# Optimization experiments

Measured on AMD Instinct MI355X. Metric: run time of the kernel, lower is better.

The kernel has to match this reference:

```python
import jax, jax.numpy as jnp
from jax import lax
import numpy as np

HIDDEN = 16
INPUT = 1
OUTPUT = 1
BATCH = 8192
SEQ = 512


def setup_inputs() -> dict:
    key = jax.random.key(0)
    ks = jax.random.split(key, 12)
    s = 1.0 / np.sqrt(HIDDEN)  # PyTorch nn.RNN init scale
    u = lambda k, shape: jax.random.uniform(k, shape, jnp.float32, -s, s)
    return {
        "x": jax.random.normal(ks[0], (BATCH, SEQ, INPUT), jnp.float32),
        "W_ih0": u(ks[1], (HIDDEN, INPUT)),
        "W_hh0": u(ks[2], (HIDDEN, HIDDEN)),
        "b_ih0": u(ks[3], (HIDDEN,)),
        "b_hh0": u(ks[4], (HIDDEN,)),
        "W_ih1": u(ks[5], (HIDDEN, HIDDEN)),
        "W_hh1": u(ks[6], (HIDDEN, HIDDEN)),
        "b_ih1": u(ks[7], (HIDDEN,)),
        "b_hh1": u(ks[8], (HIDDEN,)),
        "W_fc": u(ks[9], (OUTPUT, HIDDEN)),
        "b_fc": u(ks[10], (OUTPUT,)),
    }


def reference(x, W_ih0, W_hh0, b_ih0, b_hh0, W_ih1, W_hh1, b_ih1, b_hh1, W_fc, b_fc):
    # x: [B, S, input]; 2-layer tanh RNN (batch_first), zero initial state,
    # then fc applied to the last timestep of the top layer.
    B = x.shape[0]
    h_init = (jnp.zeros((B, HIDDEN), x.dtype), jnp.zeros((B, HIDDEN), x.dtype))

    def step(carry, xt):  # xt: [B, input]
        h0, h1 = carry
        h0 = jnp.tanh(xt @ W_ih0.T + b_ih0 + h0 @ W_hh0.T + b_hh0)
        h1 = jnp.tanh(h0 @ W_ih1.T + b_ih1 + h1 @ W_hh1.T + b_hh1)
        return (h0, h1), None

    xs = jnp.swapaxes(x, 0, 1)  # [S, B, input] for scan over time
    (h0, h1), _ = lax.scan(step, h_init, xs)
    return h1 @ W_fc.T + b_fc  # [B, output]
```

## Files before the change

### kernel.cpp

```cpp
#include <hip/hip_runtime.h>
#include <hip/hip_fp16.h>


typedef __fp16 f16x4 __attribute__((ext_vector_type(4)));
typedef __fp16 f16x2 __attribute__((ext_vector_type(2)));
typedef float  f32x4 __attribute__((ext_vector_type(4)));

__device__ __forceinline__ float tanh_fast(float v) {
    float e = __builtin_amdgcn_exp2f(v * 2.8853900817779268f);
    float r = __builtin_amdgcn_rcpf(e + 1.0f);
    return fmaf(-2.0f, r, 1.0f);
}

__global__ __launch_bounds__(64, 1) void rnn2_mfma(
    const float* __restrict__ x,
    const float* __restrict__ Wih0, const float* __restrict__ Whh0,
    const float* __restrict__ bih0, const float* __restrict__ bhh0,
    const float* __restrict__ Wih1, const float* __restrict__ Whh1,
    const float* __restrict__ bih1, const float* __restrict__ bhh1,
    const float* __restrict__ Wfc,  const float* __restrict__ bfc,
    float* __restrict__ out)
{
    const int lane = threadIdx.x & 63;
    const int q    = lane >> 4;
    const int col  = lane & 15;
    const int m4   = q * 4;
    const int b0   = blockIdx.x * 16;

    f16x4 Ahh0, Aih1, Ahh1;
#pragma unroll
    for (int i = 0; i < 4; ++i) {
        Ahh0[i] = (__fp16)Whh0[col * 16 + m4 + i];
        Aih1[i] = (__fp16)Wih1[col * 16 + m4 + i];
        Ahh1[i] = (__fp16)Whh1[col * 16 + m4 + i];
    }
    float wih0q[4], b0q[4], wfcq[4];
    f32x4 cb1;
#pragma unroll
    for (int r = 0; r < 4; ++r) {
        wih0q[r] = Wih0[m4 + r];
        b0q[r]   = bih0[m4 + r] + bhh0[m4 + r];
        cb1[r]   = bih1[m4 + r] + bhh1[m4 + r];
        wfcq[r]  = Wfc[m4 + r];
    }
    const float* __restrict__ xrow = x + (size_t)(b0 + col) * 512;

    f16x4 Bh0 = {0, 0, 0, 0}, Bh1 = {0, 0, 0, 0};
    const f32x4 zero4 = {0.f, 0.f, 0.f, 0.f};
    float u0 = 0.f, u1 = 0.f, u2 = 0.f, u3 = 0.f;

    float xc[16], xn[16];
#pragma unroll
    for (int i = 0; i < 16; ++i) xc[i] = xrow[i];

    for (int t0 = 0; t0 < 512; t0 += 16) {
        const int tn = (t0 + 16) & 511;
#pragma unroll
        for (int i = 0; i < 16; ++i) xn[i] = xrow[tn + i];

#pragma unroll
        for (int j = 0; j < 16; ++j) {
            const float xt = xc[j];
            f32x4 c0;
            c0[0] = fmaf(wih0q[0], xt, b0q[0]);
            c0[1] = fmaf(wih0q[1], xt, b0q[1]);
            c0[2] = fmaf(wih0q[2], xt, b0q[2]);
            c0[3] = fmaf(wih0q[3], xt, b0q[3]);

            f32x4 a = __builtin_amdgcn_mfma_f32_16x16x16f16(Ahh0, Bh0, c0, 0, 0, 0);
            const float s0 = tanh_fast(a[0]);
            const float s1 = tanh_fast(a[1]);
            const float s2 = tanh_fast(a[2]);
            const float s3 = tanh_fast(a[3]);
            f16x2 p0 = __builtin_amdgcn_cvt_pkrtz(s0, s1);
            f16x2 p1 = __builtin_amdgcn_cvt_pkrtz(s2, s3);
            Bh0 = __builtin_shufflevector(p0, p1, 0, 1, 2, 3);

            f32x4 d = __builtin_amdgcn_mfma_f32_16x16x16f16(Aih1, Bh0, cb1, 0, 0, 0);
            f32x4 e = __builtin_amdgcn_mfma_f32_16x16x16f16(Ahh1, Bh1, zero4, 0, 0, 0);
            u0 = tanh_fast(d[0] + e[0]);
            u1 = tanh_fast(d[1] + e[1]);
            u2 = tanh_fast(d[2] + e[2]);
            u3 = tanh_fast(d[3] + e[3]);
            f16x2 r0 = __builtin_amdgcn_cvt_pkrtz(u0, u1);
            f16x2 r1 = __builtin_amdgcn_cvt_pkrtz(u2, u3);
            Bh1 = __builtin_shufflevector(r0, r1, 0, 1, 2, 3);
        }
#pragma unroll
        for (int i = 0; i < 16; ++i) xc[i] = xn[i];
    }

    float v = u0 * wfcq[0] + u1 * wfcq[1] + u2 * wfcq[2] + u3 * wfcq[3];
    v += __shfl_xor(v, 16, 64);
    v += __shfl_xor(v, 32, 64);
    if (lane < 16) out[b0 + lane] = v + bfc[0];
}

extern "C" void kernel_launch(void* const* d_in, const int* in_sizes, int n_in,
                              void* d_out, int out_size, void* d_ws, size_t ws_size,
                              hipStream_t stream) {
    const float* x    = (const float*)d_in[0];
    const float* Wih0 = (const float*)d_in[1];
    const float* Whh0 = (const float*)d_in[2];
    const float* bih0 = (const float*)d_in[3];
    const float* bhh0 = (const float*)d_in[4];
    const float* Wih1 = (const float*)d_in[5];
    const float* Whh1 = (const float*)d_in[6];
    const float* bih1 = (const float*)d_in[7];
    const float* bhh1 = (const float*)d_in[8];
    const float* Wfc  = (const float*)d_in[9];
    const float* bfc  = (const float*)d_in[10];
    float* out = (float*)d_out;

    rnn2_mfma<<<dim3(512), dim3(64), 0, stream>>>(
        x, Wih0, Whh0, bih0, bhh0, Wih1, Whh1, bih1, bhh1, Wfc, bfc, out);
}
```

Baseline: 172.1 us.

## Skew layer-0 recurrence one timestep ahead of layer 1 to overlap MFMA chains

Layer 0's hidden state for the first timestep is computed in a prologue. Each loop iteration then computes layer 0 for step t+1 and layer 1 for step t from the same h0_t. This makes the three MFMAs in an iteration independent, so the serial chain per timestep drops from two MFMA-plus-tanh stages to one. The last iteration does one wasted layer-0 step on a wrapped x value. The cost is slightly higher register pressure to hold both sets of tanh inputs.

```diff
diff --git a/kernel.cpp b/kernel.cpp
--- a/kernel.cpp
+++ b/kernel.cpp
@@ -45,13 +45,50 @@
     }
     const float* __restrict__ xrow = x + (size_t)(b0 + col) * 512;
 
-    f16x4 Bh0 = {0, 0, 0, 0}, Bh1 = {0, 0, 0, 0};
     const f32x4 zero4 = {0.f, 0.f, 0.f, 0.f};
+    f16x4 Bh0, Bh1 = {0, 0, 0, 0};
     float u0 = 0.f, u1 = 0.f, u2 = 0.f, u3 = 0.f;
 
     float xc[16], xn[16];
 #pragma unroll
     for (int i = 0; i < 16; ++i) xc[i] = xrow[i];
+
+    {
+        const float xt = xc[0];
+        const float s0 = tanh_fast(fmaf(wih0q[0], xt, b0q[0]));
+        const float s1 = tanh_fast(fmaf(wih0q[1], xt, b0q[1]));
+        const float s2 = tanh_fast(fmaf(wih0q[2], xt, b0q[2]));
+        const float s3 = tanh_fast(fmaf(wih0q[3], xt, b0q[3]));
+        f16x2 p0 = __builtin_amdgcn_cvt_pkrtz(s0, s1);
+        f16x2 p1 = __builtin_amdgcn_cvt_pkrtz(s2, s3);
+        Bh0 = __builtin_shufflevector(p0, p1, 0, 1, 2, 3);
+    }
+
+#define STEP(xt1)                                                             \
+  {                                                                           \
+    f32x4 c0;                                                                 \
+    c0[0] = fmaf(wih0q[0], (xt1), b0q[0]);                                    \
+    c0[1] = fmaf(wih0q[1], (xt1), b0q[1]);                                    \
+    c0[2] = fmaf(wih0q[2], (xt1), b0q[2]);                                    \
+    c0[3] = fmaf(wih0q[3], (xt1), b0q[3]);                                    \
+    f32x4 a = __builtin_amdgcn_mfma_f32_16x16x16f16(Ahh0, Bh0, c0, 0, 0, 0);  \
+    f32x4 d = __builtin_amdgcn_mfma_f32_16x16x16f16(Aih1, Bh0, cb1, 0, 0, 0); \
+    f32x4 e = __builtin_amdgcn_mfma_f32_16x16x16f16(Ahh1, Bh1, zero4, 0, 0, 0);\
+    u0 = tanh_fast(d[0] + e[0]);                                              \
+    u1 = tanh_fast(d[1] + e[1]);                                              \
+    u2 = tanh_fast(d[2] + e[2]);                                              \
+    u3 = tanh_fast(d[3] + e[3]);                                              \
+    f16x2 r0 = __builtin_amdgcn_cvt_pkrtz(u0, u1);                            \
+    f16x2 r1 = __builtin_amdgcn_cvt_pkrtz(u2, u3);                            \
+    Bh1 = __builtin_shufflevector(r0, r1, 0, 1, 2, 3);                        \
+    const float s0 = tanh_fast(a[0]);                                         \
+    const float s1 = tanh_fast(a[1]);                                         \
+    const float s2 = tanh_fast(a[2]);                                         \
+    const float s3 = tanh_fast(a[3]);                                         \
+    f16x2 p0 = __builtin_amdgcn_cvt_pkrtz(s0, s1);                            \
+    f16x2 p1 = __builtin_amdgcn_cvt_pkrtz(s2, s3);                            \
+    Bh0 = __builtin_shufflevector(p0, p1, 0, 1, 2, 3);                        \
+  }
 
     for (int t0 = 0; t0 < 512; t0 += 16) {
         const int tn = (t0 + 16) & 511;
@@ -60,31 +97,8 @@
 
 #pragma unroll
         for (int j = 0; j < 16; ++j) {
-            const float xt = xc[j];
-            f32x4 c0;
-            c0[0] = fmaf(wih0q[0], xt, b0q[0]);
-            c0[1] = fmaf(wih0q[1], xt, b0q[1]);
-            c0[2] = fmaf(wih0q[2], xt, b0q[2]);
-            c0[3] = fmaf(wih0q[3], xt, b0q[3]);
-
-            f32x4 a = __builtin_amdgcn_mfma_f32_16x16x16f16(Ahh0, Bh0, c0, 0, 0, 0);
-            const float s0 = tanh_fast(a[0]);
-            const float s1 = tanh_fast(a[1]);
-            const float s2 = tanh_fast(a[2]);
-            const float s3 = tanh_fast(a[3]);
-            f16x2 p0 = __builtin_amdgcn_cvt_pkrtz(s0, s1);
-            f16x2 p1 = __builtin_amdgcn_cvt_pkrtz(s2, s3);
-            Bh0 = __builtin_shufflevector(p0, p1, 0, 1, 2, 3);
-
-            f32x4 d = __builtin_amdgcn_mfma_f32_16x16x16f16(Aih1, Bh0, cb1, 0, 0, 0);
-            f32x4 e = __builtin_amdgcn_mfma_f32_16x16x16f16(Ahh1, Bh1, zero4, 0, 0, 0);
-            u0 = tanh_fast(d[0] + e[0]);
-            u1 = tanh_fast(d[1] + e[1]);
-            u2 = tanh_fast(d[2] + e[2]);
-            u3 = tanh_fast(d[3] + e[3]);
-            f16x2 r0 = __builtin_amdgcn_cvt_pkrtz(u0, u1);
-            f16x2 r1 = __builtin_amdgcn_cvt_pkrtz(u2, u3);
-            Bh1 = __builtin_shufflevector(r0, r1, 0, 1, 2, 3);
+            const float xt1 = (j < 15) ? xc[j + 1] : xn[0];
+            STEP(xt1)
         }
 #pragma unroll
         for (int i = 0; i < 16; ++i) xc[i] = xn[i];
```

Result: faster. 164.5 us (-4.4%).

## Interleave two batch tiles per wave and skew layer-0 one step ahead

Applied to the files above, without the earlier changes.

Each wave now handles two independent 16-row batch tiles, with their MFMA and tanh chains interleaved so one tile's dependent latency is hidden by the other's work. The layer-0 recurrence is also skewed one timestep ahead through a prologue, so the layer-0 and both layer-1 MFMAs for a step can issue together. The grid halves to 256 blocks of one wave each, which leaves fewer waves on a 256-CU device, and register pressure rises.

```diff
diff --git a/kernel.cpp b/kernel.cpp
--- a/kernel.cpp
+++ b/kernel.cpp
@@ -12,7 +12,7 @@
     return fmaf(-2.0f, r, 1.0f);
 }
 
-__global__ __launch_bounds__(64, 1) void rnn2_mfma(
+__global__ __launch_bounds__(64, 1) void rnn2_mfma2(
     const float* __restrict__ x,
     const float* __restrict__ Wih0, const float* __restrict__ Whh0,
     const float* __restrict__ bih0, const float* __restrict__ bhh0,
@@ -25,7 +25,8 @@
     const int q    = lane >> 4;
     const int col  = lane & 15;
     const int m4   = q * 4;
-    const int b0   = blockIdx.x * 16;
+    const int b0A  = blockIdx.x * 32;
+    const int b0B  = b0A + 16;
 
     f16x4 Ahh0, Aih1, Ahh1;
 #pragma unroll
@@ -43,57 +44,88 @@
         cb1[r]   = bih1[m4 + r] + bhh1[m4 + r];
         wfcq[r]  = Wfc[m4 + r];
     }
-    const float* __restrict__ xrow = x + (size_t)(b0 + col) * 512;
+    const float* __restrict__ xrowA = x + (size_t)(b0A + col) * 512;
+    const float* __restrict__ xrowB = x + (size_t)(b0B + col) * 512;
 
-    f16x4 Bh0 = {0, 0, 0, 0}, Bh1 = {0, 0, 0, 0};
     const f32x4 zero4 = {0.f, 0.f, 0.f, 0.f};
-    float u0 = 0.f, u1 = 0.f, u2 = 0.f, u3 = 0.f;
+    f16x4 Bh0A, Bh1A = {0, 0, 0, 0}, Bh0B, Bh1B = {0, 0, 0, 0};
+    float uA0 = 0.f, uA1 = 0.f, uA2 = 0.f, uA3 = 0.f;
+    float uB0 = 0.f, uB1 = 0.f, uB2 = 0.f, uB3 = 0.f;
 
-    float xc[16], xn[16];
+#define PROLOG(SFX, xrow)                                                     \
+  {                                                                           \
+    const float xt = (xrow)[0];                                               \
+    const float s0 = tanh_fast(fmaf(wih0q[0], xt, b0q[0]));                   \
+    const float s1 = tanh_fast(fmaf(wih0q[1], xt, b0q[1]));                   \
+    const float s2 = tanh_fast(fmaf(wih0q[2], xt, b0q[2]));                   \
+    const float s3 = tanh_fast(fmaf(wih0q[3], xt, b0q[3]));                   \
+    f16x2 p0 = __builtin_amdgcn_cvt_pkrtz(s0, s1);                            \
+    f16x2 p1 = __builtin_amdgcn_cvt_pkrtz(s2, s3);                            \
+    Bh0##SFX = __builtin_shufflevector(p0, p1, 0, 1, 2, 3);                   \
+  }
+    PROLOG(A, xrowA)
+    PROLOG(B, xrowB)
+
+    float xcA[8], xnA[8], xcB[8], xnB[8];
 #pragma unroll
-    for (int i = 0; i < 16; ++i) xc[i] = xrow[i];
+    for (int i = 0; i < 8; ++i) { xcA[i] = xrowA[1 + i]; xcB[i] = xrowB[1 + i]; }
 
-    for (int t0 = 0; t0 < 512; t0 += 16) {
-        const int tn = (t0 + 16) & 511;
+#define STEP_MM(SFX, xt1)                                                     \
+    f32x4 c0##SFX;                                                            \
+    c0##SFX[0] = fmaf(wih0q[0], (xt1), b0q[0]);                               \
+    c0##SFX[1] = fmaf(wih0q[1], (xt1), b0q[1]);                               \
+    c0##SFX[2] = fmaf(wih0q[2], (xt1), b0q[2]);                               \
+    c0##SFX[3] = fmaf(wih0q[3], (xt1), b0q[3]);                               \
+    f32x4 a##SFX = __builtin_amdgcn_mfma_f32_16x16x16f16(Ahh0, Bh0##SFX, c0##SFX, 0, 0, 0); \
+    f32x4 d##SFX = __builtin_amdgcn_mfma_f32_16x16x16f16(Aih1, Bh0##SFX, cb1, 0, 0, 0);     \
+    f32x4 e##SFX = __builtin_amdgcn_mfma_f32_16x16x16f16(Ahh1, Bh1##SFX, zero4, 0, 0, 0);
+
+#define STEP_TANH(SFX)                                                        \
+    u##SFX##0 = tanh_fast(d##SFX[0] + e##SFX[0]);                             \
+    u##SFX##1 = tanh_fast(d##SFX[1] + e##SFX[1]);                             \
+    u##SFX##2 = tanh_fast(d##SFX[2] + e##SFX[2]);                             \
+    u##SFX##3 = tanh_fast(d##SFX[3] + e##SFX[3]);                             \
+    {                                                                         \
+      f16x2 r0 = __builtin_amdgcn_cvt_pkrtz(u##SFX##0, u##SFX##1);            \
+      f16x2 r1 = __builtin_amdgcn_cvt_pkrtz(u##SFX##2, u##SFX##3);            \
+      Bh1##SFX = __builtin_shufflevector(r0, r1, 0, 1, 2, 3);                 \
+      const float s0 = tanh_fast(a##SFX[0]);                                  \
+      const float s1 = tanh_fast(a##SFX[1]);                                  \
+      const float s2 = tanh_fast(a##SFX[2]);                                  \
+      const float s3 = tanh_fast(a##SFX[3]);                                  \
+      f16x2 p0 = __builtin_amdgcn_cvt_pkrtz(s0, s1);                          \
+      f16x2 p1 = __builtin_amdgcn_cvt_pkrtz(s2, s3);                          \
+      Bh0##SFX = __builtin_shufflevector(p0, p1, 0, 1, 2, 3);                 \
+    }
+
+    for (int t0 = 0; t0 < 512; t0 += 8) {
 #pragma unroll
-        for (int i = 0; i < 16; ++i) xn[i] = xrow[tn + i];
-
-#pragma unroll
-        for (int j = 0; j < 16; ++j) {
-            const float xt = xc[j];
-            f32x4 c0;
-            c0[0] = fmaf(wih0q[0], xt, b0q[0]);
-            c0[1] = fmaf(wih0q[1], xt, b0q[1]);
-            c0[2] = fmaf(wih0q[2], xt, b0q[2]);
-            c0[3] = fmaf(wih0q[3], xt, b0q[3]);
-
-            f32x4 a = __builtin_amdgcn_mfma_f32_16x16x16f16(Ahh0, Bh0, c0, 0, 0, 0);
-            const float s0 = tanh_fast(a[0]);
-            const float s1 = tanh_fast(a[1]);
-            const float s2 = tanh_fast(a[2]);
-            const float s3 = tanh_fast(a[3]);
-            f16x2 p0 = __builtin_amdgcn_cvt_pkrtz(s0, s1);
-            f16x2 p1 = __builtin_amdgcn_cvt_pkrtz(s2, s3);
-            Bh0 = __builtin_shufflevector(p0, p1, 0, 1, 2, 3);
-
-            f32x4 d = __builtin_amdgcn_mfma_f32_16x16x16f16(Aih1, Bh0, cb1, 0, 0, 0);
-            f32x4 e = __builtin_amdgcn_mfma_f32_16x16x16f16(Ahh1, Bh1, zero4, 0, 0, 0);
-            u0 = tanh_fast(d[0] + e[0]);
-            u1 = tanh_fast(d[1] + e[1]);
-            u2 = tanh_fast(d[2] + e[2]);
-            u3 = tanh_fast(d[3] + e[3]);
-            f16x2 r0 = __builtin_amdgcn_cvt_pkrtz(u0, u1);
-            f16x2 r1 = __builtin_amdgcn_cvt_pkrtz(u2, u3);
-            Bh1 = __builtin_shufflevector(r0, r1, 0, 1, 2, 3);
+        for (int i = 0; i < 8; ++i) {
+            const int tn = (t0 + 9 + i) & 511;
+            xnA[i] = xrowA[tn];
+            xnB[i] = xrowB[tn];
         }
 #pragma unroll
-        for (int i = 0; i < 16; ++i) xc[i] = xn[i];
+        for (int j = 0; j < 8; ++j) {
+            STEP_MM(A, xcA[j])
+            STEP_MM(B, xcB[j])
+            STEP_TANH(A)
+            STEP_TANH(B)
+        }
+#pragma unroll
+        for (int i = 0; i < 8; ++i) { xcA[i] = xnA[i]; xcB[i] = xnB[i]; }
     }
 
-    float v = u0 * wfcq[0] + u1 * wfcq[1] + u2 * wfcq[2] + u3 * wfcq[3];
-    v += __shfl_xor(v, 16, 64);
-    v += __shfl_xor(v, 32, 64);
-    if (lane < 16) out[b0 + lane] = v + bfc[0];
+    float vA = uA0 * wfcq[0] + uA1 * wfcq[1] + uA2 * wfcq[2] + uA3 * wfcq[3];
+    float vB = uB0 * wfcq[0] + uB1 * wfcq[1] + uB2 * wfcq[2] + uB3 * wfcq[3];
+    vA += __shfl_xor(vA, 16, 64);
+    vA += __shfl_xor(vA, 32, 64);
+    vB += __shfl_xor(vB, 16, 64);
+    vB += __shfl_xor(vB, 32, 64);
+    if (lane < 16) {
+        out[b0A + lane] = vA + bfc[0];
+        out[b0B + lane] = vB + bfc[0];
+    }
 }
 
 extern "C" void kernel_launch(void* const* d_in, const int* in_sizes, int n_in,
@@ -112,6 +144,6 @@
     const float* bfc  = (const float*)d_in[10];
     float* out = (float*)d_out;
 
-    rnn2_mfma<<<dim3(512), dim3(64), 0, stream>>>(
+    rnn2_mfma2<<<dim3(256), dim3(64), 0, stream>>>(
         x, Wih0, Whh0, bih0, bhh0, Wih1, Whh1, bih1, bhh1, Wfc, bfc, out);
 }
```

After: 241.8 us. +40.5%, slower.

## Split RNN layers across two wavefronts pipelined through shared memory

Applied to the files above, without the earlier changes.

The two RNN layers now run on separate wavefronts within a 128-thread block. Wave 0 computes layer 0 one step ahead and passes h0 through a 4-slot LDS ring, while wave 1 computes layer 1, which shortens each wave's serial dependency chain. The cost is a __syncthreads barrier every timestep plus LDS traffic, which may offset the overlap gained.

```diff
diff --git a/kernel.cpp b/kernel.cpp
--- a/kernel.cpp
+++ b/kernel.cpp
@@ -12,7 +12,7 @@
     return fmaf(-2.0f, r, 1.0f);
 }
 
-__global__ __launch_bounds__(64, 1) void rnn2_mfma(
+__global__ __launch_bounds__(128, 1) void rnn2_pipe(
     const float* __restrict__ x,
     const float* __restrict__ Wih0, const float* __restrict__ Whh0,
     const float* __restrict__ bih0, const float* __restrict__ bhh0,
@@ -21,11 +21,15 @@
     const float* __restrict__ Wfc,  const float* __restrict__ bfc,
     float* __restrict__ out)
 {
-    const int lane = threadIdx.x & 63;
+    const int tid  = threadIdx.x;
+    const int wid  = tid >> 6;
+    const int lane = tid & 63;
     const int q    = lane >> 4;
     const int col  = lane & 15;
     const int m4   = q * 4;
     const int b0   = blockIdx.x * 16;
+
+    __shared__ unsigned long long h0slot[4][64];
 
     f16x4 Ahh0, Aih1, Ahh1;
 #pragma unroll
@@ -44,56 +48,92 @@
         wfcq[r]  = Wfc[m4 + r];
     }
     const float* __restrict__ xrow = x + (size_t)(b0 + col) * 512;
+    const f32x4 zero4 = {0.f, 0.f, 0.f, 0.f};
 
-    f16x4 Bh0 = {0, 0, 0, 0}, Bh1 = {0, 0, 0, 0};
-    const f32x4 zero4 = {0.f, 0.f, 0.f, 0.f};
+    f16x4 Bh0;
+    float xc[16], xn[16];
+    f16x4 h0cur, Bh1 = {0, 0, 0, 0};
+    unsigned long long h0nxt = 0;
     float u0 = 0.f, u1 = 0.f, u2 = 0.f, u3 = 0.f;
 
-    float xc[16], xn[16];
+    if (wid == 0) {
+        {
+            const float x0 = xrow[0];
+            f16x2 p0 = __builtin_amdgcn_cvt_pkrtz(
+                tanh_fast(fmaf(wih0q[0], x0, b0q[0])),
+                tanh_fast(fmaf(wih0q[1], x0, b0q[1])));
+            f16x2 p1 = __builtin_amdgcn_cvt_pkrtz(
+                tanh_fast(fmaf(wih0q[2], x0, b0q[2])),
+                tanh_fast(fmaf(wih0q[3], x0, b0q[3])));
+            Bh0 = __builtin_shufflevector(p0, p1, 0, 1, 2, 3);
+        }
+        h0slot[0][lane] = __builtin_bit_cast(unsigned long long, Bh0);
+        {
+            const float x1 = xrow[1];
+            f32x4 c0;
+            c0[0] = fmaf(wih0q[0], x1, b0q[0]);
+            c0[1] = fmaf(wih0q[1], x1, b0q[1]);
+            c0[2] = fmaf(wih0q[2], x1, b0q[2]);
+            c0[3] = fmaf(wih0q[3], x1, b0q[3]);
+            f32x4 a = __builtin_amdgcn_mfma_f32_16x16x16f16(Ahh0, Bh0, c0, 0, 0, 0);
+            f16x2 p0 = __builtin_amdgcn_cvt_pkrtz(tanh_fast(a[0]), tanh_fast(a[1]));
+            f16x2 p1 = __builtin_amdgcn_cvt_pkrtz(tanh_fast(a[2]), tanh_fast(a[3]));
+            Bh0 = __builtin_shufflevector(p0, p1, 0, 1, 2, 3);
+        }
+        h0slot[1][lane] = __builtin_bit_cast(unsigned long long, Bh0);
 #pragma unroll
-    for (int i = 0; i < 16; ++i) xc[i] = xrow[i];
+        for (int i = 0; i < 16; ++i) xc[i] = xrow[(2 + i) & 511];
+    }
+    __syncthreads();
+    if (wid == 1) h0cur = __builtin_bit_cast(f16x4, h0slot[0][lane]);
 
     for (int t0 = 0; t0 < 512; t0 += 16) {
-        const int tn = (t0 + 16) & 511;
+        if (wid == 0) {
 #pragma unroll
-        for (int i = 0; i < 16; ++i) xn[i] = xrow[tn + i];
-
+            for (int i = 0; i < 16; ++i) xn[i] = xrow[(t0 + 18 + i) & 511];
+        }
 #pragma unroll
         for (int j = 0; j < 16; ++j) {
-            const float xt = xc[j];
-            f32x4 c0;
-            c0[0] = fmaf(wih0q[0], xt, b0q[0]);
-            c0[1] = fmaf(wih0q[1], xt, b0q[1]);
-            c0[2] = fmaf(wih0q[2], xt, b0q[2]);
-            c0[3] = fmaf(wih0q[3], xt, b0q[3]);
-
-            f32x4 a = __builtin_amdgcn_mfma_f32_16x16x16f16(Ahh0, Bh0, c0, 0, 0, 0);
-            const float s0 = tanh_fast(a[0]);
-            const float s1 = tanh_fast(a[1]);
-            const float s2 = tanh_fast(a[2]);
-            const float s3 = tanh_fast(a[3]);
-            f16x2 p0 = __builtin_amdgcn_cvt_pkrtz(s0, s1);
-            f16x2 p1 = __builtin_amdgcn_cvt_pkrtz(s2, s3);
-            Bh0 = __builtin_shufflevector(p0, p1, 0, 1, 2, 3);
-
-            f32x4 d = __builtin_amdgcn_mfma_f32_16x16x16f16(Aih1, Bh0, cb1, 0, 0, 0);
-            f32x4 e = __builtin_amdgcn_mfma_f32_16x16x16f16(Ahh1, Bh1, zero4, 0, 0, 0);
-            u0 = tanh_fast(d[0] + e[0]);
-            u1 = tanh_fast(d[1] + e[1]);
-            u2 = tanh_fast(d[2] + e[2]);
-            u3 = tanh_fast(d[3] + e[3]);
-            f16x2 r0 = __builtin_amdgcn_cvt_pkrtz(u0, u1);
-            f16x2 r1 = __builtin_amdgcn_cvt_pkrtz(u2, u3);
-            Bh1 = __builtin_shufflevector(r0, r1, 0, 1, 2, 3);
+            const int s = t0 + j;
+            if (wid == 0) {
+                const float xt = xc[j];
+                f32x4 c0;
+                c0[0] = fmaf(wih0q[0], xt, b0q[0]);
+                c0[1] = fmaf(wih0q[1], xt, b0q[1]);
+                c0[2] = fmaf(wih0q[2], xt, b0q[2]);
+                c0[3] = fmaf(wih0q[3], xt, b0q[3]);
+                f32x4 a = __builtin_amdgcn_mfma_f32_16x16x16f16(Ahh0, Bh0, c0, 0, 0, 0);
+                f16x2 p0 = __builtin_amdgcn_cvt_pkrtz(tanh_fast(a[0]), tanh_fast(a[1]));
+                f16x2 p1 = __builtin_amdgcn_cvt_pkrtz(tanh_fast(a[2]), tanh_fast(a[3]));
+                Bh0 = __builtin_shufflevector(p0, p1, 0, 1, 2, 3);
+                h0slot[(s + 2) & 3][lane] = __builtin_bit_cast(unsigned long long, Bh0);
+            } else {
+                h0nxt = h0slot[(s + 1) & 3][lane];
+                f32x4 d = __builtin_amdgcn_mfma_f32_16x16x16f16(Aih1, h0cur, cb1, 0, 0, 0);
+                f32x4 e = __builtin_amdgcn_mfma_f32_16x16x16f16(Ahh1, Bh1, zero4, 0, 0, 0);
+                u0 = tanh_fast(d[0] + e[0]);
+                u1 = tanh_fast(d[1] + e[1]);
+                u2 = tanh_fast(d[2] + e[2]);
+                u3 = tanh_fast(d[3] + e[3]);
+                f16x2 r0 = __builtin_amdgcn_cvt_pkrtz(u0, u1);
+                f16x2 r1 = __builtin_amdgcn_cvt_pkrtz(u2, u3);
+                Bh1 = __builtin_shufflevector(r0, r1, 0, 1, 2, 3);
+                h0cur = __builtin_bit_cast(f16x4, h0nxt);
+            }
+            __syncthreads();
         }
+        if (wid == 0) {
 #pragma unroll
-        for (int i = 0; i < 16; ++i) xc[i] = xn[i];
+            for (int i = 0; i < 16; ++i) xc[i] = xn[i];
+        }
     }
 
-    float v = u0 * wfcq[0] + u1 * wfcq[1] + u2 * wfcq[2] + u3 * wfcq[3];
-    v += __shfl_xor(v, 16, 64);
-    v += __shfl_xor(v, 32, 64);
-    if (lane < 16) out[b0 + lane] = v + bfc[0];
+    if (wid == 1) {
+        float v = u0 * wfcq[0] + u1 * wfcq[1] + u2 * wfcq[2] + u3 * wfcq[3];
+        v += __shfl_xor(v, 16, 64);
+        v += __shfl_xor(v, 32, 64);
+        if (lane < 16) out[b0 + lane] = v + bfc[0];
+    }
 }
 
 extern "C" void kernel_launch(void* const* d_in, const int* in_sizes, int n_in,
@@ -112,6 +152,6 @@
     const float* bfc  = (const float*)d_in[10];
     float* out = (float*)d_out;
 
-    rnn2_mfma<<<dim3(512), dim3(64), 0, stream>>>(
+    rnn2_pipe<<<dim3(512), dim3(128), 0, stream>>>(
         x, Wih0, Whh0, bih0, bhh0, Wih1, Whh1, bih1, bhh1, Wfc, bfc, out);
 }
```

Measured after the change: 197.6 us. 14.8% more time.
